# Optimization experiments

Measured on AMD Instinct MI355X. Metric: run time of the kernel, lower is better.

## Reference

```python
import jax, jax.numpy as jnp
import numpy as np

B, N, T, D = 256, 12, 20, 512
EPS_A = 1e-6          # adjacency row-sum epsilon (matches torch code)
EPS_BN = 1e-5         # BatchNorm2d default eps
DIST_THRESH = 150.0   # pixel distance threshold for graph edges


def setup_inputs() -> dict:
    key = jax.random.key(0)
    ks = jax.random.split(key, 16)
    person_features = jax.random.normal(ks[0], (B, N, T, D), dtype=jnp.float32)
    # bboxes: (x, y, w, h) in pixel coordinates of a 1280x720 frame
    bboxes = jax.random.uniform(ks[1], (B, N, 4), dtype=jnp.float32) \
             * jnp.array([1280.0, 720.0, 120.0, 200.0], dtype=jnp.float32)
    inp = {"person_features": person_features, "bboxes": bboxes}
    # STGCN layer params: 1x1 conv == per-node linear [D_out, D_in], plus BN affine + running stats
    for li in (1, 2):
        k = jax.random.split(ks[1 + li], 6)
        inp[f"W{li}"] = jax.random.normal(k[0], (D, D), dtype=jnp.float32) * (1.0 / np.sqrt(D))
        inp[f"b{li}"] = jax.random.normal(k[1], (D,), dtype=jnp.float32) * 0.01
        inp[f"g{li}"] = jnp.ones((D,), dtype=jnp.float32) + 0.1 * jax.random.normal(k[2], (D,), dtype=jnp.float32)
        inp[f"beta{li}"] = 0.1 * jax.random.normal(k[3], (D,), dtype=jnp.float32)
        inp[f"m{li}"] = 0.1 * jax.random.normal(k[4], (D,), dtype=jnp.float32)
        inp[f"v{li}"] = 0.5 + jax.random.uniform(k[5], (D,), dtype=jnp.float32)
    return inp


def _stgcn(x, A_norm, W, b, g, beta, m, v):
    # x: [B, N, C]; A_norm: [B, N, N] row-normalized adjacency
    # torch: out[c, j] = sum_n x[n, c] * A_norm[n, j]
    xg = jnp.einsum('bnc,bnj->bjc', x, A_norm)           # graph aggregation
    y = xg @ W.T + b                                      # 1x1 conv over channels
    y = g * (y - m) * jax.lax.rsqrt(v + EPS_BN) + beta    # BatchNorm2d (inference)
    return jax.nn.relu(y)


def reference(person_features, bboxes, W1, b1, g1, beta1, m1, v1,
              W2, b2, g2, beta2, m2, v2):
    # box centers: (x + w/2, y + h/2)  -> [B, N, 2]
    centers = jnp.stack([bboxes[..., 0] + bboxes[..., 2] * 0.5,
                         bboxes[..., 1] + bboxes[..., 3] * 0.5], axis=-1)
    # squared pairwise distance (threshold on d^2 avoids sqrt-at-zero); diag d=0<150 -> 1,
    # identical to off-diag threshold + added identity in the torch code.
    diff = centers[:, :, None, :] - centers[:, None, :, :]   # [B, N, N, 2]
    d2 = jnp.sum(diff * diff, axis=-1)                       # [B, N, N]
    A = (d2 < DIST_THRESH * DIST_THRESH).astype(jnp.float32)
    A_norm = A / (jnp.sum(A, axis=-1, keepdims=True) + EPS_A)

    x = person_features[:, :, -1, :]                         # last timestep [B, N, D]
    x = _stgcn(x, A_norm, W1, b1, g1, beta1, m1, v1)
    x = _stgcn(x, A_norm, W2, b2, g2, beta2, m2, v2)
    # write enhanced features back into the last timestep
    return person_features.at[:, :, -1, :].set(x)
```

## Files before the change

kernel.cpp:

```cpp
#include <hip/hip_runtime.h>

#define BB 256
#define NP 12
#define TT 20
#define DD 512
#define EPS_A 1e-6f
#define EPS_BN 1e-5f
#define THR2 (150.0f * 150.0f)
#define APITCH 520
#define COPY_TOTAL 7864320L
#define C0 491520L
#define NCPY 1792

typedef __attribute__((ext_vector_type(8))) short shortx8;
typedef __attribute__((ext_vector_type(4))) float floatx4;

static __device__ __forceinline__ ushort f2bf(float f) {
    unsigned x = __float_as_uint(f);
    return (ushort)((x + 0x7fffu + ((x >> 16) & 1u)) >> 16);
}

static __device__ __forceinline__ void copy_body(int cb, int ncb, long lo, long hi,
                                                 const float4* __restrict__ src,
                                                 float4* __restrict__ dst) {
    long stride = (long)ncb * 256;
    for (long g = lo + (long)cb * 256 + threadIdx.x; g < hi; g += stride) {
        int row = (int)(g >> 7);
        if (row % TT == TT - 1) continue;
        dst[g] = src[g];
    }
}

__global__ __launch_bounds__(256) void k_prep(
    const float* __restrict__ W1, const float* __restrict__ W2,
    const float* __restrict__ b1, const float* __restrict__ g1,
    const float* __restrict__ beta1, const float* __restrict__ m1, const float* __restrict__ v1,
    const float* __restrict__ b2, const float* __restrict__ g2,
    const float* __restrict__ beta2, const float* __restrict__ m2, const float* __restrict__ v2,
    float* __restrict__ s1, float* __restrict__ t1, float* __restrict__ s2, float* __restrict__ t2,
    ushort* __restrict__ wb1, ushort* __restrict__ wb2,
    const float4* __restrict__ csrc, float4* __restrict__ cdst) {
    int bid = blockIdx.x, t = threadIdx.x;
    if (bid < 64) {
        int idx = bid * 256 + t;
        for (int i = idx; i < 131072; i += 16384) {
            float4 f = (i < 65536) ? ((const float4*)W1)[i] : ((const float4*)W2)[i - 65536];
            ushort4 u;
            u.x = f2bf(f.x); u.y = f2bf(f.y); u.z = f2bf(f.z); u.w = f2bf(f.w);
            if (i < 65536) *(ushort4*)(wb1 + (long)i * 4) = u;
            else           *(ushort4*)(wb2 + (long)(i - 65536) * 4) = u;
        }
    } else if (bid == 64) {
        for (int d = t; d < DD; d += 256) {
            float sa = g1[d] * rsqrtf(v1[d] + EPS_BN);
            s1[d] = sa; t1[d] = (b1[d] - m1[d]) * sa + beta1[d];
            float sb = g2[d] * rsqrtf(v2[d] + EPS_BN);
            s2[d] = sb; t2[d] = (b2[d] - m2[d]) * sb + beta2[d];
        }
    } else {
        copy_body(bid - 65, 191, 0L, C0, csrc, cdst);
    }
}

template <int LAYER>
static __device__ __forceinline__ void gemm16(
    int wave, int lane, int b,
    const ushort (*__restrict__ xgl)[APITCH], float (*__restrict__ y1l)[DD],
    const ushort* __restrict__ wb, const float* __restrict__ sv, const float* __restrict__ tv,
    float* __restrict__ outp) {
    int mrow = lane & 15, quad = lane >> 4;
    floatx4 acc[8];
    #pragma unroll
    for (int nt = 0; nt < 8; nt++) acc[nt] = (floatx4){0.f, 0.f, 0.f, 0.f};

    const ushort* wbase = wb + ((long)(wave * 128 + mrow)) * DD + quad * 8;
    #pragma unroll 2
    for (int kc = 0; kc < DD; kc += 32) {
        shortx8 af = *(const shortx8*)&xgl[mrow][kc + quad * 8];
        #pragma unroll
        for (int nt = 0; nt < 8; nt++) {
            shortx8 bf = *(const shortx8*)(wbase + nt * 16 * DD + kc);
            acc[nt] = __builtin_amdgcn_mfma_f32_16x16x32_bf16(af, bf, acc[nt], 0, 0, 0);
        }
    }

    #pragma unroll
    for (int nt = 0; nt < 8; nt++) {
        int d = wave * 128 + nt * 16 + mrow;
        float s = sv[d], tt = tv[d];
        #pragma unroll
        for (int v = 0; v < 4; v++) {
            int m = quad * 4 + v;
            float val = fmaxf(acc[nt][v] * s + tt, 0.f);
            if (m < NP) {
                if (LAYER == 1) y1l[m][d] = val;
                else outp[((long)(b * NP + m) * TT + TT - 1) * DD + d] = val;
            }
        }
    }
}

__global__ __launch_bounds__(256) void k_fused(
    const float* __restrict__ pf, const float* __restrict__ bboxes,
    const ushort* __restrict__ wb1, const ushort* __restrict__ wb2,
    const float* __restrict__ s1, const float* __restrict__ t1,
    const float* __restrict__ s2, const float* __restrict__ t2,
    float* __restrict__ out,
    const float4* __restrict__ csrc, float4* __restrict__ cdst) {
    __shared__ float cx[NP], cy[NP], Ash[NP][NP], rinv[NP], at[NP][NP];
    __shared__ __align__(16) ushort xgl[16][APITCH];
    __shared__ float y1l[NP][DD];

    int bid = blockIdx.x, t = threadIdx.x;
    if (bid >= BB) {
        copy_body(bid - BB, NCPY, C0, COPY_TOTAL, csrc, cdst);
        return;
    }

    int b = bid;
    int lane = t & 63, wave = t >> 6;

    if (t < NP) {
        const float* p = bboxes + (b * NP + t) * 4;
        cx[t] = p[0] + 0.5f * p[2];
        cy[t] = p[1] + 0.5f * p[3];
    }
    {
        uint* xz = (uint*)&xgl[NP][0];
        for (int i = t; i < 4 * APITCH / 2; i += 256) xz[i] = 0;
    }
    __syncthreads();
    if (t < NP * NP) {
        int n = t / NP, k = t % NP;
        float dx = cx[n] - cx[k], dy = cy[n] - cy[k];
        Ash[n][k] = (dx * dx + dy * dy < THR2) ? 1.f : 0.f;
    }
    __syncthreads();
    if (t < NP) {
        float s = 0.f;
        #pragma unroll
        for (int k = 0; k < NP; k++) s += Ash[t][k];
        rinv[t] = 1.f / (s + EPS_A);
    }
    __syncthreads();
    if (t < NP * NP) {
        int j = t / NP, n = t % NP;
        at[j][n] = Ash[n][j] * rinv[n];
    }
    __syncthreads();

    for (int c = t; c < DD; c += 256) {
        float xv[NP];
        #pragma unroll
        for (int n = 0; n < NP; n++)
            xv[n] = pf[((long)((b * NP + n) * TT + TT - 1)) * DD + c];
        #pragma unroll
        for (int j = 0; j < NP; j++) {
            float a = 0.f;
            #pragma unroll
            for (int n = 0; n < NP; n++) a += at[j][n] * xv[n];
            xgl[j][c] = f2bf(a);
        }
    }
    __syncthreads();

    gemm16<1>(wave, lane, b, xgl, y1l, wb1, s1, t1, nullptr);
    __syncthreads();

    for (int c = t; c < DD; c += 256) {
        float xv[NP];
        #pragma unroll
        for (int n = 0; n < NP; n++) xv[n] = y1l[n][c];
        #pragma unroll
        for (int j = 0; j < NP; j++) {
            float a = 0.f;
            #pragma unroll
            for (int n = 0; n < NP; n++) a += at[j][n] * xv[n];
            xgl[j][c] = f2bf(a);
        }
    }
    __syncthreads();

    gemm16<2>(wave, lane, b, xgl, y1l, wb2, s2, t2, out);
}

extern "C" void kernel_launch(void* const* d_in, const int* in_sizes, int n_in,
                              void* d_out, int out_size, void* d_ws, size_t ws_size,
                              hipStream_t stream) {
    const float* pf = (const float*)d_in[0];
    const float* bboxes = (const float*)d_in[1];
    const float* W1 = (const float*)d_in[2];
    const float* b1 = (const float*)d_in[3];
    const float* g1 = (const float*)d_in[4];
    const float* beta1 = (const float*)d_in[5];
    const float* m1 = (const float*)d_in[6];
    const float* v1 = (const float*)d_in[7];
    const float* W2 = (const float*)d_in[8];
    const float* b2 = (const float*)d_in[9];
    const float* g2 = (const float*)d_in[10];
    const float* beta2 = (const float*)d_in[11];
    const float* m2 = (const float*)d_in[12];
    const float* v2 = (const float*)d_in[13];
    float* out = (float*)d_out;

    float* ws = (float*)d_ws;
    float* s1 = ws;
    float* t1v = ws + 512;
    float* s2 = ws + 1024;
    float* t2v = ws + 1536;
    ushort* wb1 = (ushort*)(ws + 2048);
    ushort* wb2 = wb1 + 262144;

    const float4* csrc = (const float4*)pf;
    float4* cdst = (float4*)out;

    k_prep<<<256, 256, 0, stream>>>(W1, W2, b1, g1, beta1, m1, v1,
                                    b2, g2, beta2, m2, v2,
                                    s1, t1v, s2, t2v, wb1, wb2, csrc, cdst);
    k_fused<<<BB + NCPY, 256, 0, stream>>>(pf, bboxes, wb1, wb2,
                                           s1, t1v, s2, t2v, out, csrc, cdst);
}
```

Baseline: 285.5 us.

## Rebalance copy across kernels, vectorize copy to skip last-step rows, use 8-wave compute blocks

The pass-through copy of all non-last timesteps is now indexed directly over the 19-of-20 timestep slices, with 8 float4 per thread and no per-element row test. Most of the copy moves into the first kernel (2016 blocks), and only a small share overlaps with the compute kernel. The compute kernel now uses 512 threads, so each of 8 waves computes 64 output columns with fewer accumulators. The aim is to cut wasted copy iterations, raise memory-level parallelism and shorten the MFMA critical path per block. The cost is more work in the prep kernel before compute can start, and a launch-bound change that may affect register allocation.

```diff
diff --git a/kernel.cpp b/kernel.cpp
--- a/kernel.cpp
+++ b/kernel.cpp
@@ -8,9 +8,11 @@
 #define EPS_BN 1e-5f
 #define THR2 (150.0f * 150.0f)
 #define APITCH 520
-#define COPY_TOTAL 7864320L
-#define C0 491520L
-#define NCPY 1792
+#define NSLICE 2432u
+#define TOTALC 7471104u
+#define CSPLIT 2990080u
+#define NCOPY1 2016
+#define NCOPY2 256
 
 typedef __attribute__((ext_vector_type(8))) short shortx8;
 typedef __attribute__((ext_vector_type(4))) float floatx4;
@@ -20,18 +22,22 @@
     return (ushort)((x + 0x7fffu + ((x >> 16) & 1u)) >> 16);
 }
 
-static __device__ __forceinline__ void copy_body(int cb, int ncb, long lo, long hi,
+static __device__ __forceinline__ void copy_span(uint lo, uint hi, uint tid, uint cb,
+                                                 uint ncb, uint tpb,
                                                  const float4* __restrict__ src,
                                                  float4* __restrict__ dst) {
-    long stride = (long)ncb * 256;
-    for (long g = lo + (long)cb * 256 + threadIdx.x; g < hi; g += stride) {
-        int row = (int)(g >> 7);
-        if (row % TT == TT - 1) continue;
-        dst[g] = src[g];
-    }
-}
-
-__global__ __launch_bounds__(256) void k_prep(
+    uint step = ncb * tpb * 8u;
+    for (uint i0 = lo + (cb * tpb + tid) * 8u; i0 < hi; i0 += step) {
+        uint g = i0 / NSLICE;
+        uint idx = i0 + g * 128u;
+        float4 v0 = src[idx + 0], v1 = src[idx + 1], v2 = src[idx + 2], v3 = src[idx + 3];
+        float4 v4 = src[idx + 4], v5 = src[idx + 5], v6 = src[idx + 6], v7 = src[idx + 7];
+        dst[idx + 0] = v0; dst[idx + 1] = v1; dst[idx + 2] = v2; dst[idx + 3] = v3;
+        dst[idx + 4] = v4; dst[idx + 5] = v5; dst[idx + 6] = v6; dst[idx + 7] = v7;
+    }
+}
+
+__global__ __launch_bounds__(256) void k_copyprep(
     const float* __restrict__ W1, const float* __restrict__ W2,
     const float* __restrict__ b1, const float* __restrict__ g1,
     const float* __restrict__ beta1, const float* __restrict__ m1, const float* __restrict__ v1,
@@ -43,6 +49,7 @@
     int bid = blockIdx.x, t = threadIdx.x;
     if (bid < 64) {
         int idx = bid * 256 + t;
+        #pragma unroll 2
         for (int i = idx; i < 131072; i += 16384) {
             float4 f = (i < 65536) ? ((const float4*)W1)[i] : ((const float4*)W2)[i - 65536];
             ushort4 u;
@@ -58,35 +65,35 @@
             s2[d] = sb; t2[d] = (b2[d] - m2[d]) * sb + beta2[d];
         }
     } else {
-        copy_body(bid - 65, 191, 0L, C0, csrc, cdst);
+        copy_span(CSPLIT, TOTALC, t, bid - 65, NCOPY1, 256, csrc, cdst);
     }
 }
 
 template <int LAYER>
-static __device__ __forceinline__ void gemm16(
+static __device__ __forceinline__ void gemm8w(
     int wave, int lane, int b,
     const ushort (*__restrict__ xgl)[APITCH], float (*__restrict__ y1l)[DD],
     const ushort* __restrict__ wb, const float* __restrict__ sv, const float* __restrict__ tv,
     float* __restrict__ outp) {
     int mrow = lane & 15, quad = lane >> 4;
-    floatx4 acc[8];
+    floatx4 acc[4];
     #pragma unroll
-    for (int nt = 0; nt < 8; nt++) acc[nt] = (floatx4){0.f, 0.f, 0.f, 0.f};
-
-    const ushort* wbase = wb + ((long)(wave * 128 + mrow)) * DD + quad * 8;
-    #pragma unroll 2
+    for (int nt = 0; nt < 4; nt++) acc[nt] = (floatx4){0.f, 0.f, 0.f, 0.f};
+
+    const ushort* wbase = wb + ((long)(wave * 64 + mrow)) * DD + quad * 8;
+    #pragma unroll 4
     for (int kc = 0; kc < DD; kc += 32) {
         shortx8 af = *(const shortx8*)&xgl[mrow][kc + quad * 8];
         #pragma unroll
-        for (int nt = 0; nt < 8; nt++) {
+        for (int nt = 0; nt < 4; nt++) {
             shortx8 bf = *(const shortx8*)(wbase + nt * 16 * DD + kc);
             acc[nt] = __builtin_amdgcn_mfma_f32_16x16x32_bf16(af, bf, acc[nt], 0, 0, 0);
         }
     }
 
     #pragma unroll
-    for (int nt = 0; nt < 8; nt++) {
-        int d = wave * 128 + nt * 16 + mrow;
+    for (int nt = 0; nt < 4; nt++) {
+        int d = wave * 64 + nt * 16 + mrow;
         float s = sv[d], tt = tv[d];
         #pragma unroll
         for (int v = 0; v < 4; v++) {
@@ -94,13 +101,13 @@
             float val = fmaxf(acc[nt][v] * s + tt, 0.f);
             if (m < NP) {
                 if (LAYER == 1) y1l[m][d] = val;
-                else outp[((long)(b * NP + m) * TT + TT - 1) * DD + d] = val;
+                else outp[((long)(b * NP + m) * TT + (TT - 1)) * DD + d] = val;
             }
         }
     }
 }
 
-__global__ __launch_bounds__(256) void k_fused(
+__global__ __launch_bounds__(512, 4) void k_compute(
     const float* __restrict__ pf, const float* __restrict__ bboxes,
     const ushort* __restrict__ wb1, const ushort* __restrict__ wb2,
     const float* __restrict__ s1, const float* __restrict__ t1,
@@ -113,7 +120,7 @@
 
     int bid = blockIdx.x, t = threadIdx.x;
     if (bid >= BB) {
-        copy_body(bid - BB, NCPY, C0, COPY_TOTAL, csrc, cdst);
+        copy_span(0u, CSPLIT, t, bid - BB, NCOPY2, 512, csrc, cdst);
         return;
     }
 
@@ -127,7 +134,7 @@
     }
     {
         uint* xz = (uint*)&xgl[NP][0];
-        for (int i = t; i < 4 * APITCH / 2; i += 256) xz[i] = 0;
+        for (int i = t; i < 4 * APITCH / 2; i += 512) xz[i] = 0;
     }
     __syncthreads();
     if (t < NP * NP) {
@@ -149,7 +156,7 @@
     }
     __syncthreads();
 
-    for (int c = t; c < DD; c += 256) {
+    for (int c = t; c < DD; c += 512) {
         float xv[NP];
         #pragma unroll
         for (int n = 0; n < NP; n++)
@@ -164,10 +171,10 @@
     }
     __syncthreads();
 
-    gemm16<1>(wave, lane, b, xgl, y1l, wb1, s1, t1, nullptr);
-    __syncthreads();
-
-    for (int c = t; c < DD; c += 256) {
+    gemm8w<1>(wave, lane, b, xgl, y1l, wb1, s1, t1, nullptr);
+    __syncthreads();
+
+    for (int c = t; c < DD; c += 512) {
         float xv[NP];
         #pragma unroll
         for (int n = 0; n < NP; n++) xv[n] = y1l[n][c];
@@ -181,7 +188,7 @@
     }
     __syncthreads();
 
-    gemm16<2>(wave, lane, b, xgl, y1l, wb2, s2, t2, out);
+    gemm8w<2>(wave, lane, b, xgl, y1l, wb2, s2, t2, out);
 }
 
 extern "C" void kernel_launch(void* const* d_in, const int* in_sizes, int n_in,
@@ -214,9 +221,9 @@
     const float4* csrc = (const float4*)pf;
     float4* cdst = (float4*)out;
 
-    k_prep<<<256, 256, 0, stream>>>(W1, W2, b1, g1, beta1, m1, v1,
-                                    b2, g2, beta2, m2, v2,
-                                    s1, t1v, s2, t2v, wb1, wb2, csrc, cdst);
-    k_fused<<<BB + NCPY, 256, 0, stream>>>(pf, bboxes, wb1, wb2,
-                                           s1, t1v, s2, t2v, out, csrc, cdst);
-}
+    k_copyprep<<<65 + NCOPY1, 256, 0, stream>>>(W1, W2, b1, g1, beta1, m1, v1,
+                                                b2, g2, beta2, m2, v2,
+                                                s1, t1v, s2, t2v, wb1, wb2, csrc, cdst);
+    k_compute<<<BB + NCOPY2, 512, 0, stream>>>(pf, bboxes, wb1, wb2,
+                                               s1, t1v, s2, t2v, out, csrc, cdst);
+}
```

New measurement: 293.1 us. 1.03x slower.
